# Kernel optimization log

Hardware: AMD Instinct MI355X
Metric: run time of the kernel (lower is better)

The kernel has to match this reference:

```python
import jax, jax.numpy as jnp
import numpy as np

N_GENE = 100000
N_DIS = 20000
H = 128
E = 500000


def setup_inputs() -> dict:
    key = jax.random.key(0)
    ks = jax.random.split(key, 12)
    s1 = 1.0 / np.sqrt(2 * H)  # fan-in init scale, Linear(2H, H)
    s2 = 1.0 / np.sqrt(H)      # fan-in init scale, Linear(H, 1)
    z_gene = jax.random.normal(ks[0], (N_GENE, H), jnp.float32)
    z_disease = jax.random.normal(ks[1], (N_DIS, H), jnp.float32)
    # gene->disease edges: row indexes genes, col indexes diseases
    edges_gd = jnp.stack([
        jax.random.randint(ks[2], (E,), 0, N_GENE),
        jax.random.randint(ks[3], (E,), 0, N_DIS),
    ])
    # gene->gene edges
    edges_gg = jnp.stack([
        jax.random.randint(ks[4], (E,), 0, N_GENE),
        jax.random.randint(ks[5], (E,), 0, N_GENE),
    ])
    return {
        "z_gene": z_gene,
        "z_disease": z_disease,
        "edges_gd": edges_gd,
        "edges_gg": edges_gg,
        "w1_gd": jax.random.normal(ks[6], (2 * H, H), jnp.float32) * s1,
        "b1_gd": jnp.zeros((H,), jnp.float32),
        "w2_gd": jax.random.normal(ks[7], (H, 1), jnp.float32) * s2,
        "b2_gd": jnp.zeros((1,), jnp.float32),
        "w1_gg": jax.random.normal(ks[8], (2 * H, H), jnp.float32) * s1,
        "b1_gg": jnp.zeros((H,), jnp.float32),
        "w2_gg": jax.random.normal(ks[9], (H, 1), jnp.float32) * s2,
        "b2_gg": jnp.zeros((1,), jnp.float32),
    }


def _decode(z_src, z_dst, edges, w1, b1, w2, b2):
    # gather src/dst node embeddings by edge index, concat -> [E, 2H]
    z = jnp.concatenate([z_src[edges[0]], z_dst[edges[1]]], axis=1)
    h = jnp.maximum(z @ w1 + b1, 0.0)  # Linear + ReLU
    return h @ w2 + b2                  # Linear -> [E, 1]


def reference(z_gene, z_disease, edges_gd, edges_gg,
              w1_gd, b1_gd, w2_gd, b2_gd,
              w1_gg, b1_gg, w2_gg, b2_gg):
    out_gd = _decode(z_gene, z_disease, edges_gd, w1_gd, b1_gd, w2_gd, b2_gd)
    out_gg = _decode(z_gene, z_gene, edges_gg, w1_gg, b1_gg, w2_gg, b2_gg)
    # dict of per-relation outputs in the original; stack since E matches
    return jnp.stack([out_gd, out_gg])  # [2, E, 1]
```

## Files before the change

### kernel.cpp

```cpp
#include <hip/hip_runtime.h>
#include <hip/hip_bf16.h>

#define HDIM 128

typedef __attribute__((ext_vector_type(8))) short short8;
typedef __attribute__((ext_vector_type(4))) float floatx4;

__device__ __forceinline__ float bf2f(unsigned short u) {
    return __uint_as_float(((unsigned)u) << 16);
}
__device__ __forceinline__ unsigned short f2b(float f) {
    __hip_bfloat16 h = __float2bfloat16(f);
    return __builtin_bit_cast(unsigned short, h);
}
__device__ __forceinline__ float ldv(const void* p, size_t i, int flag) {
    return flag ? bf2f(((const unsigned short*)p)[i]) : ((const float*)p)[i];
}
__device__ __forceinline__ short8 pack8(float4 a, float4 b) {
    short8 r;
    r[0] = (short)f2b(a.x); r[1] = (short)f2b(a.y);
    r[2] = (short)f2b(a.z); r[3] = (short)f2b(a.w);
    r[4] = (short)f2b(b.x); r[5] = (short)f2b(b.y);
    r[6] = (short)f2b(b.z); r[7] = (short)f2b(b.w);
    return r;
}

__device__ __forceinline__ int local_detect_s(const unsigned short* zbits, int* red) {
    int tid = threadIdx.x;
    int nthr = blockDim.x;
    int cnt = 0;
    for (int i = tid; i < 4096; i += nthr) {
        int ex = (zbits[i] >> 7) & 0xFF;
        if (ex >= 100 && ex <= 140) cnt++;
    }
    red[tid] = cnt;
    __syncthreads();
    for (int s = nthr >> 1; s > 0; s >>= 1) {
        if (tid < s) red[tid] += red[tid + s];
        __syncthreads();
    }
    int f = (red[0] >= 3686) ? 1 : 0;
    __syncthreads();
    return f;
}

__device__ __forceinline__ int local_detect(const unsigned short* zbits) {
    __shared__ int red[256];
    return local_detect_s(zbits, red);
}

__global__ __launch_bounds__(256) void prep_kernel(
    const void* __restrict__ Zg, const void* __restrict__ Zd,
    const void* __restrict__ w1_gd, const void* __restrict__ w1_gg,
    const void* __restrict__ b1_gd, const void* __restrict__ w2_gd,
    const void* __restrict__ b2_gd, const void* __restrict__ b1_gg,
    const void* __restrict__ w2_gg, const void* __restrict__ b2_gg,
    unsigned short* __restrict__ img, float* __restrict__ params,
    int* __restrict__ flagout,
    unsigned short* __restrict__ Zcg, unsigned short* __restrict__ Zcd,
    int NG, int ND)
{
    int flag = local_detect((const unsigned short*)Zg);
    int b = blockIdx.x;
    int tid = threadIdx.x;
    if (b < 32) {
        int im   = b >> 3;
        int sub  = b & 7;
        const void* w1 = (im < 2) ? w1_gd : w1_gg;
        int part = im & 1;
        unsigned short* out = img + im * 16384;
        int n = tid & 127;
#pragma unroll
        for (int it = 0; it < 8; ++it) {
            int k = sub * 16 + it * 2 + (tid >> 7);
            unsigned short v = flag
                ? ((const unsigned short*)w1)[(size_t)(part * 128 + k) * 128 + n]
                : f2b(((const float*)w1)[(size_t)(part * 128 + k) * 128 + n]);
            out[n * 128 + (((k >> 3) ^ (n & 15)) << 3) + (k & 7)] = v;
        }
    } else if (b == 32) {
        if (tid < 128) {
            params[tid]       = ldv(b1_gd, tid, flag);
            params[256 + tid] = ldv(b1_gg, tid, flag);
        } else {
            params[tid]       = ldv(w2_gd, tid - 128, flag);
            params[256 + tid] = ldv(w2_gg, tid - 128, flag);
        }
        if (tid == 0) {
            params[512] = ldv(b2_gd, 0, flag);
            params[513] = ldv(b2_gg, 0, flag);
            *flagout = flag;
        }
    } else {
        if (flag) return;
        long ng8 = (long)NG * 16;
        long tot = ng8 + (long)ND * 16;
        long stride = (long)(gridDim.x - 33) * 256;
        for (long g = (long)(b - 33) * 256 + tid; g < tot; g += stride) {
            const float* srcf;
            unsigned short* dstp;
            long off;
            if (g < ng8) { srcf = (const float*)Zg; dstp = Zcg; off = g * 8; }
            else         { srcf = (const float*)Zd; dstp = Zcd; off = (g - ng8) * 8; }
            float4 f0 = *(const float4*)(srcf + off);
            float4 f1 = *(const float4*)(srcf + off + 4);
            short8 v = pack8(f0, f1);
            *(uint4*)(dstp + off) = __builtin_bit_cast(uint4, v);
        }
    }
}

__global__ __launch_bounds__(512, 2) void fused_edge_kernel(
    const void* __restrict__ Zg, const void* __restrict__ Zd,
    const unsigned short* __restrict__ Zcg, const unsigned short* __restrict__ Zcd,
    const int* __restrict__ edges_gd, const int* __restrict__ edges_gg,
    const uint4* __restrict__ Wimg, const float* __restrict__ params,
    void* __restrict__ out, int E, int nbe, const int* __restrict__ flagp)
{
    __shared__ uint4 sW[4096];
    int tid  = threadIdx.x;
    int lane = tid & 63;
    int wave = tid >> 6;
    int nl   = lane & 15;
    int quad = lane >> 4;
    int flag = *flagp;

    int rel = ((int)blockIdx.x >= nbe) ? 1 : 0;
    int blk = blockIdx.x - rel * nbe;
    const int* edges = rel ? edges_gg : edges_gd;

    const unsigned short* Tg = flag ? (const unsigned short*)Zg : Zcg;
    const unsigned short* Td = flag ? (const unsigned short*)Zd : Zcd;
    const unsigned short* Tdst = rel ? Tg : Td;

    int e  = blk * 128 + wave * 16 + nl;
    int ec = e < E ? e : E - 1;
    int src = edges[ec];
    int dst = edges[E + ec];

    short8 zf[8];
    {
        const uint4* zs = (const uint4*)Tg   + (size_t)src * 16;
        const uint4* zd = (const uint4*)Tdst + (size_t)dst * 16;
#pragma unroll
        for (int kc = 0; kc < 4; ++kc) {
            zf[kc]     = __builtin_bit_cast(short8, zs[kc * 4 + quad]);
            zf[kc + 4] = __builtin_bit_cast(short8, zd[kc * 4 + quad]);
        }
    }

    const uint4* im = Wimg + rel * 4096;
#pragma unroll
    for (int i = 0; i < 8; ++i) sW[tid + i * 512] = im[tid + i * 512];

    __syncthreads();

    floatx4 acc[8];
#pragma unroll
    for (int nt = 0; nt < 8; ++nt) acc[nt] = (floatx4){0.f, 0.f, 0.f, 0.f};

#pragma unroll
    for (int kc = 0; kc < 8; ++kc) {
        const uint4* base = sW + (kc >> 2) * 2048;
        int p = ((kc & 3) * 4 + quad) ^ nl;
#pragma unroll
        for (int nt = 0; nt < 8; ++nt) {
            short8 wf = __builtin_bit_cast(short8, base[(nt * 16 + nl) * 16 + p]);
            acc[nt] = __builtin_amdgcn_mfma_f32_16x16x32_bf16(wf, zf[kc], acc[nt], 0, 0, 0);
        }
    }

    const float* pr = params + rel * 256;
    float b2 = params[512 + rel];
    float s = 0.f;
#pragma unroll
    for (int nt = 0; nt < 8; ++nt) {
        float4 b1v = *(const float4*)(pr + nt * 16 + quad * 4);
        float4 w2v = *(const float4*)(pr + 128 + nt * 16 + quad * 4);
        s = fmaf(fmaxf(acc[nt][0] + b1v.x, 0.f), w2v.x, s);
        s = fmaf(fmaxf(acc[nt][1] + b1v.y, 0.f), w2v.y, s);
        s = fmaf(fmaxf(acc[nt][2] + b1v.z, 0.f), w2v.z, s);
        s = fmaf(fmaxf(acc[nt][3] + b1v.w, 0.f), w2v.w, s);
    }
    s += __shfl_xor(s, 16);
    s += __shfl_xor(s, 32);

    if (quad == 0 && e < E) {
        float r = s + b2;
        size_t base = (size_t)rel * E;
        if (flag) ((unsigned short*)out)[base + e] = f2b(r);
        else      ((float*)out)[base + e] = r;
    }
}

__global__ __launch_bounds__(256) void detect_kernel(
    const unsigned short* __restrict__ zbits, int* __restrict__ flag)
{
    int f = local_detect(zbits);
    if (threadIdx.x == 0) *flag = f;
}

__global__ __launch_bounds__(128) void naive_edge_kernel(
    const int* __restrict__ edges,
    const void* __restrict__ zsrc, const void* __restrict__ zdst,
    const void* __restrict__ w1, const void* __restrict__ b1,
    const void* __restrict__ w2, const void* __restrict__ b2,
    void* __restrict__ out, size_t eoff, int E,
    const int* __restrict__ flagp)
{
    int flag = flagp ? *flagp : 0;
    __shared__ float zs[128], zd[128], red[128];
    int e = blockIdx.x;
    int n = threadIdx.x;
    int src = edges[e], dst = edges[E + e];
    zs[n] = ldv(zsrc, (size_t)src * HDIM + n, flag);
    zd[n] = ldv(zdst, (size_t)dst * HDIM + n, flag);
    __syncthreads();
    float acc = ldv(b1, n, flag);
    for (int k = 0; k < 128; ++k) acc = fmaf(zs[k], ldv(w1, (size_t)k * HDIM + n, flag), acc);
    for (int k = 0; k < 128; ++k) acc = fmaf(zd[k], ldv(w1, (size_t)(128 + k) * HDIM + n, flag), acc);
    red[n] = fmaxf(acc, 0.f) * ldv(w2, n, flag);
    __syncthreads();
    for (int s = 64; s > 0; s >>= 1) {
        if (n < s) red[n] += red[n + s];
        __syncthreads();
    }
    if (n == 0) {
        float r = red[0] + ldv(b2, 0, flag);
        if (flag) ((unsigned short*)out)[eoff + e] = f2b(r);
        else      ((float*)out)[eoff + e] = r;
    }
}

extern "C" void kernel_launch(void* const* d_in, const int* in_sizes, int n_in,
                              void* d_out, int out_size, void* d_ws, size_t ws_size,
                              hipStream_t stream)
{
    const void* z_gene = d_in[0];
    const void* z_dis  = d_in[1];
    const int* edges_gd = (const int*)d_in[2];
    const int* edges_gg = (const int*)d_in[3];
    const void* w1_gd = d_in[4];
    const void* b1_gd = d_in[5];
    const void* w2_gd = d_in[6];
    const void* b2_gd = d_in[7];
    const void* w1_gg = d_in[8];
    const void* b1_gg = d_in[9];
    const void* w2_gg = d_in[10];
    const void* b2_gg = d_in[11];

    int NG = in_sizes[0] / HDIM;
    int ND = in_sizes[1] / HDIM;
    int E  = in_sizes[2] / 2;

    size_t off_flag   = 0;
    size_t off_params = 256;
    size_t off_img    = 2560;
    size_t off_Zcg    = off_img + 131072;
    size_t off_Zcd    = off_Zcg + (size_t)NG * HDIM * 2;
    size_t need       = off_Zcd + (size_t)ND * HDIM * 2;

    char* ws = (char*)d_ws;

    if (ws_size < need) {
        const int* flagp = nullptr;
        if (ws_size >= 16) {
            detect_kernel<<<1, 256, 0, stream>>>((const unsigned short*)z_gene, (int*)ws);
            flagp = (const int*)ws;
        }
        naive_edge_kernel<<<E, 128, 0, stream>>>(edges_gd, z_gene, z_dis,
                                                 w1_gd, b1_gd, w2_gd, b2_gd,
                                                 d_out, 0, E, flagp);
        naive_edge_kernel<<<E, 128, 0, stream>>>(edges_gg, z_gene, z_gene,
                                                 w1_gg, b1_gg, w2_gg, b2_gg,
                                                 d_out, (size_t)E, E, flagp);
        return;
    }

    int* flag = (int*)(ws + off_flag);
    float* params = (float*)(ws + off_params);
    unsigned short* img = (unsigned short*)(ws + off_img);
    unsigned short* Zcg = (unsigned short*)(ws + off_Zcg);
    unsigned short* Zcd = (unsigned short*)(ws + off_Zcd);

    prep_kernel<<<33 + 512, 256, 0, stream>>>(
        z_gene, z_dis,
        w1_gd, w1_gg, b1_gd, w2_gd, b2_gd, b1_gg, w2_gg, b2_gg,
        img, params, flag, Zcg, Zcd, NG, ND);

    int nbe = (E + 127) / 128;
    fused_edge_kernel<<<2 * nbe, 512, 0, stream>>>(
        z_gene, z_dis, Zcg, Zcd, edges_gd, edges_gg,
        (const uint4*)img, params, d_out, E, nbe, flag);
}
```

Measured before the change: 228.0 us.

## Split weight staging into two N-halves to cut LDS and raise occupancy

The 64KB shared-memory weight tile is replaced by a 32KB buffer. Each half of the hidden dimension is loaded and consumed in turn, with only four accumulators live per half. Launch bounds rise from 2 to 8 blocks per CU, so more edge-gather waves can be resident to hide the latency of the random embedding reads. The cost is an extra pair of block barriers and reloading half the weights per block, plus a tighter register budget that could cause spills.

```diff
diff --git a/kernel.cpp b/kernel.cpp
--- a/kernel.cpp
+++ b/kernel.cpp
@@ -110,14 +110,14 @@
     }
 }
 
-__global__ __launch_bounds__(512, 2) void fused_edge_kernel(
+__global__ __launch_bounds__(512, 8) void fused_edge_kernel(
     const void* __restrict__ Zg, const void* __restrict__ Zd,
     const unsigned short* __restrict__ Zcg, const unsigned short* __restrict__ Zcd,
     const int* __restrict__ edges_gd, const int* __restrict__ edges_gg,
     const uint4* __restrict__ Wimg, const float* __restrict__ params,
     void* __restrict__ out, int E, int nbe, const int* __restrict__ flagp)
 {
-    __shared__ uint4 sW[4096];
+    __shared__ uint4 sW[2048];
     int tid  = threadIdx.x;
     int lane = tid & 63;
     int wave = tid >> 6;
@@ -150,43 +150,53 @@
     }
 
     const uint4* im = Wimg + rel * 4096;
-#pragma unroll
-    for (int i = 0; i < 8; ++i) sW[tid + i * 512] = im[tid + i * 512];
-
-    __syncthreads();
-
-    floatx4 acc[8];
-#pragma unroll
-    for (int nt = 0; nt < 8; ++nt) acc[nt] = (floatx4){0.f, 0.f, 0.f, 0.f};
-
-#pragma unroll
-    for (int kc = 0; kc < 8; ++kc) {
-        const uint4* base = sW + (kc >> 2) * 2048;
-        int p = ((kc & 3) * 4 + quad) ^ nl;
-#pragma unroll
-        for (int nt = 0; nt < 8; ++nt) {
-            short8 wf = __builtin_bit_cast(short8, base[(nt * 16 + nl) * 16 + p]);
-            acc[nt] = __builtin_amdgcn_mfma_f32_16x16x32_bf16(wf, zf[kc], acc[nt], 0, 0, 0);
-        }
-    }
-
     const float* pr = params + rel * 256;
-    float b2 = params[512 + rel];
     float s = 0.f;
-#pragma unroll
-    for (int nt = 0; nt < 8; ++nt) {
-        float4 b1v = *(const float4*)(pr + nt * 16 + quad * 4);
-        float4 w2v = *(const float4*)(pr + 128 + nt * 16 + quad * 4);
-        s = fmaf(fmaxf(acc[nt][0] + b1v.x, 0.f), w2v.x, s);
-        s = fmaf(fmaxf(acc[nt][1] + b1v.y, 0.f), w2v.y, s);
-        s = fmaf(fmaxf(acc[nt][2] + b1v.z, 0.f), w2v.z, s);
-        s = fmaf(fmaxf(acc[nt][3] + b1v.w, 0.f), w2v.w, s);
-    }
+
+#pragma unroll
+    for (int c = 0; c < 2; ++c) {
+#pragma unroll
+        for (int i = 0; i < 4; ++i) {
+            int j = tid + i * 512;
+            int half = j >> 10;
+            int idx  = j & 1023;
+            sW[j] = im[half * 2048 + c * 1024 + idx];
+        }
+        __syncthreads();
+
+        floatx4 acc[4];
+#pragma unroll
+        for (int nt4 = 0; nt4 < 4; ++nt4) acc[nt4] = (floatx4){0.f, 0.f, 0.f, 0.f};
+
+#pragma unroll
+        for (int kc = 0; kc < 8; ++kc) {
+            const uint4* base = sW + (kc >> 2) * 1024;
+            int p = ((kc & 3) * 4 + quad) ^ nl;
+#pragma unroll
+            for (int nt4 = 0; nt4 < 4; ++nt4) {
+                short8 wf = __builtin_bit_cast(short8, base[(nt4 * 16 + nl) * 16 + p]);
+                acc[nt4] = __builtin_amdgcn_mfma_f32_16x16x32_bf16(wf, zf[kc], acc[nt4], 0, 0, 0);
+            }
+        }
+
+#pragma unroll
+        for (int nt4 = 0; nt4 < 4; ++nt4) {
+            int nt = c * 4 + nt4;
+            float4 b1v = *(const float4*)(pr + nt * 16 + quad * 4);
+            float4 w2v = *(const float4*)(pr + 128 + nt * 16 + quad * 4);
+            s = fmaf(fmaxf(acc[nt4][0] + b1v.x, 0.f), w2v.x, s);
+            s = fmaf(fmaxf(acc[nt4][1] + b1v.y, 0.f), w2v.y, s);
+            s = fmaf(fmaxf(acc[nt4][2] + b1v.z, 0.f), w2v.z, s);
+            s = fmaf(fmaxf(acc[nt4][3] + b1v.w, 0.f), w2v.w, s);
+        }
+        __syncthreads();
+    }
+
     s += __shfl_xor(s, 16);
     s += __shfl_xor(s, 32);
 
     if (quad == 0 && e < E) {
-        float r = s + b2;
+        float r = s + params[512 + rel];
         size_t base = (size_t)rel * E;
         if (flag) ((unsigned short*)out)[base + e] = f2b(r);
         else      ((float*)out)[base + e] = r;
```

Measured after the change: 262.8 us. 1.15x slower.
